# Optimization experiments

Measured on AMD Instinct MI355X. Metric: run time of the kernel, lower is better.

The kernel has to match this reference:

```python
import jax, jax.numpy as jnp
import numpy as np

STEPS = 8
TOL = 1e-6


def _kabsch(p, q):
    # p, q: [B, N, 3]; returns R [B,3,3], t [B,3] s.t. q ~= R p + t (pypose svdtf)
    pm = p.mean(axis=-2, keepdims=True)
    qm = q.mean(axis=-2, keepdims=True)
    pc = p - pm
    qc = q - qm
    H = jnp.einsum('bni,bnj->bij', pc, qc)          # 3x3 cross-covariance
    U, S, Vt = jnp.linalg.svd(H, full_matrices=False)
    V = jnp.swapaxes(Vt, -1, -2)
    Ut = jnp.swapaxes(U, -1, -2)
    d = jnp.linalg.det(jnp.matmul(V, Ut))            # reflection fix
    D = jnp.concatenate([jnp.ones(d.shape + (2,), d.dtype), d[..., None]], axis=-1)
    R = jnp.matmul(V * D[..., None, :], Ut)
    t = qm[..., 0, :] - jnp.einsum('bij,bj->bi', R, pm[..., 0, :])
    return R, t


def _rotmat_to_quat(R):
    # branchless rotation-matrix -> quaternion [qx, qy, qz, qw] (pypose order)
    r00, r11, r22 = R[..., 0, 0], R[..., 1, 1], R[..., 2, 2]
    qw = 0.5 * jnp.sqrt(jnp.clip(1.0 + r00 + r11 + r22, 1e-12))
    qx = 0.5 * jnp.sqrt(jnp.clip(1.0 + r00 - r11 - r22, 1e-12))
    qy = 0.5 * jnp.sqrt(jnp.clip(1.0 - r00 + r11 - r22, 1e-12))
    qz = 0.5 * jnp.sqrt(jnp.clip(1.0 - r00 - r11 + r22, 1e-12))
    qx = qx * jnp.where(R[..., 2, 1] - R[..., 1, 2] >= 0, 1.0, -1.0)
    qy = qy * jnp.where(R[..., 0, 2] - R[..., 2, 0] >= 0, 1.0, -1.0)
    qz = qz * jnp.where(R[..., 1, 0] - R[..., 0, 1] >= 0, 1.0, -1.0)
    return jnp.stack([qx, qy, qz, qw], axis=-1)


def _icp(psrc, ptgt):
    B = psrc.shape[0]
    tn = (ptgt * ptgt).sum(-1)                        # [B, M]

    def body(carry, _):
        pc, err, done = carry
        # brute-force 1-NN: Euclidean cdist via  |p|^2 + |q|^2 - 2 p.q
        sq = ((pc * pc).sum(-1)[:, :, None] + tn[:, None, :]
              - 2.0 * jnp.einsum('bnd,bmd->bnm', pc, ptgt))
        dist = jnp.sqrt(jnp.clip(sq, 0.0))            # [B, N, M]
        knnd = dist.min(axis=-1)                      # [B, N]
        idx = dist.argmin(axis=-1)                    # [B, N]
        errnew = knnd.mean(axis=-1)                   # [B]
        conv = jnp.all(jnp.abs(errnew - err) < TOL)
        done_new = jnp.logical_or(done, conv)
        qk = jnp.take_along_axis(ptgt, jnp.broadcast_to(idx[..., None], pc.shape), axis=1)
        R, t = _kabsch(pc, qk)
        pcnew = jnp.einsum('bij,bnj->bni', R, pc) + t[:, None, :]
        pc = jnp.where(done_new, pc, pcnew)
        err = jnp.where(done_new, err, errnew)
        return (pc, err, done_new), None

    init = (psrc, jnp.zeros((B,), psrc.dtype), jnp.array(False))
    (pc, _, _), _ = jax.lax.scan(body, init, None, length=STEPS)
    R, t = _kabsch(psrc, pc)                          # final fit psrc -> moved cloud
    quat = _rotmat_to_quat(R)
    return jnp.concatenate([t, quat], axis=-1)        # SE3 7-vector [t, qx,qy,qz,qw]


def setup_inputs() -> dict:
    key = jax.random.key(0)
    k1, k2 = jax.random.split(key)
    psrc = jax.random.normal(k1, (2, 4096, 3), dtype=jnp.float32)
    ptgt = jax.random.normal(k2, (2, 4096, 3), dtype=jnp.float32)
    return {"psrc": psrc, "ptgt": ptgt}


def reference(psrc, ptgt):
    return _icp(psrc, ptgt)
```

## Files before the change

### kernel.cpp

```cpp
#include <hip/hip_runtime.h>
#include <math.h>

#define NPTS 4096
#define MPTS 4096
#define NSTEPS 8
#define ICP_TOL 1e-6f
#define NBLK 512
#define NSUB 32

#define ACC_OFF 32768
#define CTR_OFF 98304
#define CTR_STRIDE 1536

__global__ void init_kernel(const float* __restrict__ ptgt, float* __restrict__ ws) {
    float* ptgt4 = ws;
    unsigned* ctrs = (unsigned*)(ws + CTR_OFF);
    int gid = blockIdx.x * 256 + threadIdx.x;
    if (gid < 2 * MPTS) {
        float x = ptgt[3 * gid + 0];
        float y = ptgt[3 * gid + 1];
        float z = ptgt[3 * gid + 2];
        float4 v;
        v.x = x; v.y = y; v.z = z;
        v.w = 0.5f * (x * x + y * y + z * z);
        ((float4*)ptgt4)[gid] = v;
    }
    for (int i = gid; i < NSTEPS * CTR_STRIDE; i += 8192) ctrs[i] = 0u;
}

__device__ __forceinline__ float frcp(float x) {
#if __has_builtin(__builtin_amdgcn_rcpf)
    return __builtin_amdgcn_rcpf(x);
#else
    return 1.f / x;
#endif
}
__device__ __forceinline__ float frsq(float x) {
#if __has_builtin(__builtin_amdgcn_rsqf)
    return __builtin_amdgcn_rsqf(x);
#else
    return 1.f / sqrtf(x);
#endif
}

#define DET3(a,b,c,d,e,f,g,h,i) \
    ((a)*((e)*(i)-(f)*(h)) - (b)*((d)*(i)-(f)*(g)) + (c)*((d)*(h)-(e)*(g)))

__device__ __forceinline__ void horn_quat(const float N[4][4], float q[4]) {
    float s = 1e-30f;
#pragma unroll
    for (int i = 0; i < 4; ++i)
#pragma unroll
        for (int j = 0; j < 4; ++j) s = fmaxf(s, fabsf(N[i][j]));
    float inv = frcp(s);
    float A[4][4], B[4][4];
#pragma unroll
    for (int i = 0; i < 4; ++i)
#pragma unroll
        for (int j = 0; j < 4; ++j) A[i][j] = N[i][j] * inv;
#pragma unroll
    for (int i = 0; i < 4; ++i)
#pragma unroll
        for (int j = i; j < 4; ++j) {
            float v = A[i][0]*A[0][j] + A[i][1]*A[1][j] + A[i][2]*A[2][j] + A[i][3]*A[3][j];
            B[i][j] = v; B[j][i] = v;
        }
    float p1 = A[0][0]+A[1][1]+A[2][2]+A[3][3];
    float p2 = B[0][0]+B[1][1]+B[2][2]+B[3][3];
    float p3 = 0.f, p4 = 0.f;
#pragma unroll
    for (int i = 0; i < 4; ++i)
#pragma unroll
        for (int j = 0; j < 4; ++j) { p3 += A[i][j]*B[i][j]; p4 += B[i][j]*B[i][j]; }
    float e1 = p1;
    float e2 = 0.5f*(e1*p1 - p2);
    float e3 = (e2*p1 - e1*p2 + p3)*(1.f/3.f);
    float e4 = 0.25f*(e3*p1 - e2*p2 + e1*p3 - p4);
    float lam = -3e38f;
#pragma unroll
    for (int i = 0; i < 4; ++i) {
        float r = A[i][i];
#pragma unroll
        for (int j = 0; j < 4; ++j) if (j != i) r += fabsf(A[i][j]);
        lam = fmaxf(lam, r);
    }
#pragma unroll
    for (int it = 0; it < 12; ++it) {
        float pv = (((lam - e1)*lam + e2)*lam - e3)*lam + e4;
        float dv = ((4.f*lam - 3.f*e1)*lam + 2.f*e2)*lam - e3;
        lam -= pv * frcp(dv);
    }
    float M[4][4];
#pragma unroll
    for (int i = 0; i < 4; ++i)
#pragma unroll
        for (int j = 0; j < 4; ++j) M[i][j] = A[i][j] - ((i == j) ? lam : 0.f);
    float C0 = DET3(M[1][1],M[1][2],M[1][3], M[2][1],M[2][2],M[2][3], M[3][1],M[3][2],M[3][3]);
    float C1 = DET3(M[0][0],M[0][2],M[0][3], M[2][0],M[2][2],M[2][3], M[3][0],M[3][2],M[3][3]);
    float C2 = DET3(M[0][0],M[0][1],M[0][3], M[1][0],M[1][1],M[1][3], M[3][0],M[3][1],M[3][3]);
    float C3 = DET3(M[0][0],M[0][1],M[0][2], M[1][0],M[1][1],M[1][2], M[2][0],M[2][1],M[2][2]);
    int is = 0; float cb = fabsf(C0);
    if (fabsf(C1) > cb) { cb = fabsf(C1); is = 1; }
    if (fabsf(C2) > cb) { cb = fabsf(C2); is = 2; }
    if (fabsf(C3) > cb) { cb = fabsf(C3); is = 3; }
    float v0, v1, v2, v3;
#define ROWCOF(a,b,c) { \
    v0 =  DET3(M[a][1],M[a][2],M[a][3], M[b][1],M[b][2],M[b][3], M[c][1],M[c][2],M[c][3]); \
    v1 = -DET3(M[a][0],M[a][2],M[a][3], M[b][0],M[b][2],M[b][3], M[c][0],M[c][2],M[c][3]); \
    v2 =  DET3(M[a][0],M[a][1],M[a][3], M[b][0],M[b][1],M[b][3], M[c][0],M[c][1],M[c][3]); \
    v3 = -DET3(M[a][0],M[a][1],M[a][2], M[b][0],M[b][1],M[b][2], M[c][0],M[c][1],M[c][2]); }
    if (is == 0)      ROWCOF(1,2,3)
    else if (is == 1) ROWCOF(0,2,3)
    else if (is == 2) ROWCOF(0,1,3)
    else              ROWCOF(0,1,2)
#undef ROWCOF
    float nr = frsq(v0*v0 + v1*v1 + v2*v2 + v3*v3);
    q[0] = v0*nr; q[1] = v1*nr; q[2] = v2*nr; q[3] = v3*nr;
}

#define FOR16(OP) OP(0) OP(1) OP(2) OP(3) OP(4) OP(5) OP(6) OP(7) \
                  OP(8) OP(9) OP(10) OP(11) OP(12) OP(13) OP(14) OP(15)

__global__ __launch_bounds__(256, 2) void icp_main(
    const float* __restrict__ psrc, float* __restrict__ ws,
    float* __restrict__ out) {

    float* ptgt4 = ws;
    float* acc = ws + ACC_OFF;
    unsigned* ctrs = (unsigned*)(ws + CTR_OFF);

    __shared__ float st[2][13];
    __shared__ unsigned keys[4][16];
    __shared__ float red[16][16];
    __shared__ float gred[16][16];
    __shared__ float asum[2][16];
    __shared__ int contflag;

    const int tid = threadIdx.x;
    const int bid = blockIdx.x;
    const int b = bid >> 8;
    const int n0 = (bid & 255) * 16;

    if (tid < 2) {
        st[tid][0] = 1.f; st[tid][1] = 0.f; st[tid][2] = 0.f;
        st[tid][3] = 0.f; st[tid][4] = 1.f; st[tid][5] = 0.f;
        st[tid][6] = 0.f; st[tid][7] = 0.f; st[tid][8] = 1.f;
        st[tid][9] = 0.f; st[tid][10] = 0.f; st[tid][11] = 0.f;
        st[tid][12] = 0.f;
    }
    __syncthreads();

    const int w = tid >> 6, lane = tid & 63;
    const int m0 = w * 1024 + lane;
    const float4* tpb = (const float4*)ptgt4 + ((size_t)b * MPTS + m0);
    const float* ps = psrc + ((size_t)b * NPTS + n0) * 3;

    for (int step = 0; step < NSTEPS; ++step) {
        float R00 = st[b][0], R01 = st[b][1], R02 = st[b][2];
        float R10 = st[b][3], R11 = st[b][4], R12 = st[b][5];
        float R20 = st[b][6], R21 = st[b][7], R22 = st[b][8];
        float t0 = st[b][9], t1 = st[b][10], t2 = st[b][11];

#define DECLP(i) float px##i, py##i, pz##i;
        FOR16(DECLP)
#undef DECLP
#define LOADP(i) { float x = ps[3*(i)], y = ps[3*(i)+1], z = ps[3*(i)+2]; \
        px##i = fmaf(R00, x, fmaf(R01, y, fmaf(R02, z, t0))); \
        py##i = fmaf(R10, x, fmaf(R11, y, fmaf(R12, z, t1))); \
        pz##i = fmaf(R20, x, fmaf(R21, y, fmaf(R22, z, t2))); }
        FOR16(LOADP)
#undef LOADP

#define DECLB(i) float bs##i = -3.0e38f; int ix##i = m0;
        FOR16(DECLB)
#undef DECLB

        float4 tc0 = tpb[0];
        float4 tc1 = tpb[64];
        int mreg = m0;
#pragma unroll
        for (int k = 0; k < 16; ++k) {
            float4 tnx = tpb[((k + 2) & 15) * 64];
            float tx = tc0.x, ty = tc0.y, tz = tc0.z, htn = tc0.w;
#define PAIR(i) { float s = fmaf(px##i, tx, fmaf(py##i, ty, fmaf(pz##i, tz, -htn))); \
            if (s > bs##i) { bs##i = s; ix##i = mreg; } }
            FOR16(PAIR)
#undef PAIR
            mreg += 64;
            tc0 = tc1;
            tc1 = tnx;
        }

        unsigned k_[16];
#define MKKEY(i) { unsigned ub = __float_as_uint(bs##i); \
        unsigned u = ((int)ub >= 0) ? (ub | 0x80000000u) : ~ub; \
        k_[i] = (u & 0xFFFFF000u) | (4095u - (unsigned)ix##i); }
        FOR16(MKKEY)
#undef MKKEY
#pragma unroll
        for (int r = 0; r < 4; ++r) {
            const int mm = 1 << r;
            const int W = 16 >> r;
            unsigned o_[16];
#pragma unroll
            for (int j = 0; j < W; ++j)
                o_[j] = (unsigned)__shfl_xor((int)k_[j], mm);
            const bool hi = (lane & mm) != 0;
#pragma unroll
            for (int j = 0; j < W / 2; ++j) {
                unsigned a = hi ? k_[j + W / 2] : k_[j];
                unsigned c = hi ? o_[j + W / 2] : o_[j];
                k_[j] = a > c ? a : c;
            }
        }
        {
            unsigned o = (unsigned)__shfl_xor((int)k_[0], 16);
            k_[0] = k_[0] > o ? k_[0] : o;
            o = (unsigned)__shfl_xor((int)k_[0], 32);
            k_[0] = k_[0] > o ? k_[0] : o;
        }
        if (lane < 16) {
            int p = ((lane & 1) << 3) | ((lane & 2) << 1) |
                    ((lane & 4) >> 1) | ((lane & 8) >> 3);
            keys[w][p] = k_[0];
        }
        __syncthreads();

        if (tid < 16) {
            unsigned key = keys[0][tid];
            unsigned k1 = keys[1][tid], k2 = keys[2][tid], k3 = keys[3][tid];
            key = key > k1 ? key : k1;
            key = key > k2 ? key : k2;
            key = key > k3 ? key : k3;
            int m = 4095 - (int)(key & 0xFFFu);
            float4 qq = ((const float4*)ptgt4)[(size_t)b * MPTS + m];
            const float* pp = psrc + ((size_t)b * NPTS + n0 + tid) * 3;
            float x = pp[0], y = pp[1], z = pp[2];
            float px = fmaf(R00, x, fmaf(R01, y, fmaf(R02, z, t0)));
            float py = fmaf(R10, x, fmaf(R11, y, fmaf(R12, z, t1)));
            float pz = fmaf(R20, x, fmaf(R21, y, fmaf(R22, z, t2)));
            float dx = px - qq.x, dy = py - qq.y, dz = pz - qq.z;
            float dist = sqrtf(dx * dx + dy * dy + dz * dz);
            red[tid][0] = px; red[tid][1] = py; red[tid][2] = pz;
            red[tid][3] = qq.x; red[tid][4] = qq.y; red[tid][5] = qq.z;
            red[tid][6] = px * qq.x;  red[tid][7] = px * qq.y;  red[tid][8] = px * qq.z;
            red[tid][9] = py * qq.x;  red[tid][10] = py * qq.y; red[tid][11] = py * qq.z;
            red[tid][12] = pz * qq.x; red[tid][13] = pz * qq.y; red[tid][14] = pz * qq.z;
            red[tid][15] = dist;
            float s = 0.f;
#pragma unroll
            for (int r = 0; r < 16; ++r) s += red[r][tid];
            __hip_atomic_store(&acc[((size_t)step * NBLK + bid) * 16 + tid], s,
                               __ATOMIC_RELAXED, __HIP_MEMORY_SCOPE_AGENT);
        }

        unsigned* stepc = ctrs + step * CTR_STRIDE;
        __syncthreads();

        if (step == NSTEPS - 1) {
            if (tid == 0) {
                unsigned* sub = stepc + (bid & (NSUB - 1)) * 16;
                unsigned old = __hip_atomic_fetch_add(sub, 1u, __ATOMIC_RELAXED,
                                                      __HIP_MEMORY_SCOPE_AGENT);
                if (old == (unsigned)(NBLK / NSUB) - 1u)
                    __hip_atomic_fetch_add(stepc + 512, 1u, __ATOMIC_RELAXED,
                                           __HIP_MEMORY_SCOPE_AGENT);
            }
            if (bid != 0) return;
            if (tid == 0) {
                while (__hip_atomic_load(stepc + 512, __ATOMIC_RELAXED,
                                         __HIP_MEMORY_SCOPE_AGENT) < (unsigned)NSUB) {
                    __builtin_amdgcn_s_sleep(1);
                }
            }
            __syncthreads();
        } else {
            if (tid == 0) {
                unsigned* sub = stepc + (bid & (NSUB - 1)) * 16;
                bool bcast = false;
                unsigned old = __hip_atomic_fetch_add(sub, 1u, __ATOMIC_RELAXED,
                                                      __HIP_MEMORY_SCOPE_AGENT);
                if (old == (unsigned)(NBLK / NSUB) - 1u) {
                    unsigned mold = __hip_atomic_fetch_add(stepc + 512, 1u,
                                        __ATOMIC_RELAXED, __HIP_MEMORY_SCOPE_AGENT);
                    if (mold == (unsigned)NSUB - 1u) {
#pragma unroll
                        for (int f = 0; f < NSUB; ++f)
                            __hip_atomic_store(stepc + 1024 + f * 16, 1u,
                                               __ATOMIC_RELAXED,
                                               __HIP_MEMORY_SCOPE_AGENT);
                        bcast = true;
                    }
                }
                if (!bcast) {
                    unsigned* myflag = stepc + 1024 + (bid & (NSUB - 1)) * 16;
                    while (__hip_atomic_load(myflag, __ATOMIC_RELAXED,
                                             __HIP_MEMORY_SCOPE_AGENT) == 0u) {
                        __builtin_amdgcn_s_sleep(1);
                    }
                }
            }
            __syncthreads();
        }

        {
            const float* accs = acc + (size_t)step * NBLK * 16;
            int c = tid & 15, g = tid >> 4;
            float ssum = 0.f;
#pragma unroll
            for (int i = 0; i < 32; ++i)
                ssum += accs[(size_t)(g * 32 + i) * 16 + c];
            gred[g][c] = ssum;
        }
        __syncthreads();
        if (tid < 32) {
            int bb = tid >> 4, c = tid & 15;
            float s = 0.f;
#pragma unroll
            for (int g = 0; g < 8; ++g) s += gred[bb * 8 + g][c];
            asum[bb][c] = s;
        }
        __syncthreads();
        if (tid == 0) {
            float err0 = asum[0][15] * (1.f / NPTS);
            float err1 = asum[1][15] * (1.f / NPTS);
            bool conv = (fabsf(err0 - st[0][12]) < ICP_TOL) &&
                        (fabsf(err1 - st[1][12]) < ICP_TOL);
            contflag = conv ? 2 : 1;
        }
        __syncthreads();
        if (contflag == 1 && tid < 2) {
            float a[16];
            for (int i = 0; i < 16; ++i) a[i] = asum[tid][i];
            const float inv_n = 1.f / NPTS;
            float pmx = a[0]*inv_n, pmy = a[1]*inv_n, pmz = a[2]*inv_n;
            float qmx = a[3]*inv_n, qmy = a[4]*inv_n, qmz = a[5]*inv_n;
            float H[3][3];
            for (int i = 0; i < 3; ++i)
                for (int j = 0; j < 3; ++j)
                    H[i][j] = a[6 + 3*i + j] - a[i]*a[3 + j]*inv_n;
            float Sxx=H[0][0], Sxy=H[0][1], Sxz=H[0][2];
            float Syx=H[1][0], Syy=H[1][1], Syz=H[1][2];
            float Szx=H[2][0], Szy=H[2][1], Szz=H[2][2];
            float Nm[4][4];
            Nm[0][0] = Sxx+Syy+Szz; Nm[0][1] = Syz-Szy;
            Nm[0][2] = Szx-Sxz;     Nm[0][3] = Sxy-Syx;
            Nm[1][1] = Sxx-Syy-Szz; Nm[1][2] = Sxy+Syx; Nm[1][3] = Szx+Sxz;
            Nm[2][2] = -Sxx+Syy-Szz; Nm[2][3] = Syz+Szy;
            Nm[3][3] = -Sxx-Syy+Szz;
            Nm[1][0]=Nm[0][1]; Nm[2][0]=Nm[0][2]; Nm[3][0]=Nm[0][3];
            Nm[2][1]=Nm[1][2]; Nm[3][1]=Nm[1][3]; Nm[3][2]=Nm[2][3];
            float qv[4];
            horn_quat(Nm, qv);
            float qw = qv[0], qx = qv[1], qy = qv[2], qz = qv[3];
            float R00n = 1.f - 2.f*(qy*qy + qz*qz);
            float R01n = 2.f*(qx*qy - qw*qz);
            float R02n = 2.f*(qx*qz + qw*qy);
            float R10n = 2.f*(qx*qy + qw*qz);
            float R11n = 1.f - 2.f*(qx*qx + qz*qz);
            float R12n = 2.f*(qy*qz - qw*qx);
            float R20n = 2.f*(qx*qz - qw*qy);
            float R21n = 2.f*(qy*qz + qw*qx);
            float R22n = 1.f - 2.f*(qx*qx + qy*qy);
            float tx = qmx - (R00n*pmx + R01n*pmy + R02n*pmz);
            float ty = qmy - (R10n*pmx + R11n*pmy + R12n*pmz);
            float tz = qmz - (R20n*pmx + R21n*pmy + R22n*pmz);
            float C00=st[tid][0], C01=st[tid][1], C02=st[tid][2];
            float C10=st[tid][3], C11=st[tid][4], C12=st[tid][5];
            float C20=st[tid][6], C21=st[tid][7], C22=st[tid][8];
            float T0=st[tid][9], T1=st[tid][10], T2=st[tid][11];
            float ns[12];
            ns[0] = R00n*C00 + R01n*C10 + R02n*C20;
            ns[1] = R00n*C01 + R01n*C11 + R02n*C21;
            ns[2] = R00n*C02 + R01n*C12 + R02n*C22;
            ns[3] = R10n*C00 + R11n*C10 + R12n*C20;
            ns[4] = R10n*C01 + R11n*C11 + R12n*C21;
            ns[5] = R10n*C02 + R11n*C12 + R12n*C22;
            ns[6] = R20n*C00 + R21n*C10 + R22n*C20;
            ns[7] = R20n*C01 + R21n*C11 + R22n*C21;
            ns[8] = R20n*C02 + R21n*C12 + R22n*C22;
            ns[9]  = R00n*T0 + R01n*T1 + R02n*T2 + tx;
            ns[10] = R10n*T0 + R11n*T1 + R12n*T2 + ty;
            ns[11] = R20n*T0 + R21n*T1 + R22n*T2 + tz;
            for (int i = 0; i < 12; ++i) st[tid][i] = ns[i];
            st[tid][12] = asum[tid][15] * (1.f / NPTS);
        }
        __syncthreads();
        if (contflag == 2) break;
    }

    if (bid == 0 && tid < 2) {
        float r00 = st[tid][0], r01 = st[tid][1], r02 = st[tid][2];
        float r10 = st[tid][3], r11 = st[tid][4], r12 = st[tid][5];
        float r20 = st[tid][6], r21 = st[tid][7], r22 = st[tid][8];
        float qw = 0.5f * sqrtf(fmaxf(1.f + r00 + r11 + r22, 1e-12f));
        float qx = 0.5f * sqrtf(fmaxf(1.f + r00 - r11 - r22, 1e-12f));
        float qy = 0.5f * sqrtf(fmaxf(1.f - r00 + r11 - r22, 1e-12f));
        float qz = 0.5f * sqrtf(fmaxf(1.f - r00 - r11 + r22, 1e-12f));
        qx = (r21 - r12 >= 0.f) ? qx : -qx;
        qy = (r02 - r20 >= 0.f) ? qy : -qy;
        qz = (r10 - r01 >= 0.f) ? qz : -qz;
        out[tid * 7 + 0] = st[tid][9];
        out[tid * 7 + 1] = st[tid][10];
        out[tid * 7 + 2] = st[tid][11];
        out[tid * 7 + 3] = qx;
        out[tid * 7 + 4] = qy;
        out[tid * 7 + 5] = qz;
        out[tid * 7 + 6] = qw;
    }
}

extern "C" void kernel_launch(void* const* d_in, const int* in_sizes, int n_in,
                              void* d_out, int out_size, void* d_ws, size_t ws_size,
                              hipStream_t stream) {
    const float* psrc = (const float*)d_in[0];
    const float* ptgt = (const float*)d_in[1];
    float* out = (float*)d_out;
    float* ws = (float*)d_ws;

    init_kernel<<<32, 256, 0, stream>>>(ptgt, ws);
    icp_main<<<NBLK, 256, 0, stream>>>(psrc, ws, out);
}
```

Before: 160.4 us.

## Per-batch pose solve per block, hoisted source loads, deeper prefetch, tree reductions

Each block now reduces only its own batch's partial sums, plus the other batch's error term for the global convergence test, and solves the Horn pose only for its own batch on one thread. Previously two threads solved both batches from a combined reduction. Source points are loaded into registers once instead of every step, the target prefetch gets one more stage, and the per-block and grid-wide reductions become two-level trees with more parallel threads. The Newton iteration count for the eigenvalue drops from 12 to 8. These changes shorten the serial tail of each step, which every block executes after the grid barrier, at the cost of extra registers and barriers and a possible small loss of eigenvalue precision.

```diff
diff --git a/kernel.cpp b/kernel.cpp
--- a/kernel.cpp
+++ b/kernel.cpp
@@ -85,7 +85,7 @@
         lam = fmaxf(lam, r);
     }
 #pragma unroll
-    for (int it = 0; it < 12; ++it) {
+    for (int it = 0; it < 8; ++it) {
         float pv = (((lam - e1)*lam + e2)*lam - e3)*lam + e4;
         float dv = ((4.f*lam - 3.f*e1)*lam + 2.f*e2)*lam - e3;
         lam -= pv * frcp(dv);
@@ -132,8 +132,14 @@
     __shared__ float st[2][13];
     __shared__ unsigned keys[4][16];
     __shared__ float red[16][16];
+    __shared__ float rq[4][16];
     __shared__ float gred[16][16];
-    __shared__ float asum[2][16];
+    __shared__ float gq[4][16];
+    __shared__ float oerr[64];
+    __shared__ float oe2[8];
+    __shared__ float asumv[16];
+    __shared__ float oerrF;
+    __shared__ float oErrPrev;
     __shared__ int contflag;
 
     const int tid = threadIdx.x;
@@ -141,12 +147,13 @@
     const int b = bid >> 8;
     const int n0 = (bid & 255) * 16;
 
-    if (tid < 2) {
-        st[tid][0] = 1.f; st[tid][1] = 0.f; st[tid][2] = 0.f;
-        st[tid][3] = 0.f; st[tid][4] = 1.f; st[tid][5] = 0.f;
-        st[tid][6] = 0.f; st[tid][7] = 0.f; st[tid][8] = 1.f;
-        st[tid][9] = 0.f; st[tid][10] = 0.f; st[tid][11] = 0.f;
-        st[tid][12] = 0.f;
+    if (tid == 0) {
+        st[b][0] = 1.f; st[b][1] = 0.f; st[b][2] = 0.f;
+        st[b][3] = 0.f; st[b][4] = 1.f; st[b][5] = 0.f;
+        st[b][6] = 0.f; st[b][7] = 0.f; st[b][8] = 1.f;
+        st[b][9] = 0.f; st[b][10] = 0.f; st[b][11] = 0.f;
+        st[b][12] = 0.f;
+        oErrPrev = 0.f;
     }
     __syncthreads();
 
@@ -154,6 +161,11 @@
     const int m0 = w * 1024 + lane;
     const float4* tpb = (const float4*)ptgt4 + ((size_t)b * MPTS + m0);
     const float* ps = psrc + ((size_t)b * NPTS + n0) * 3;
+
+    float sx[16], sy[16], sz[16];
+#define HOIST(i) { sx[i] = ps[3*(i)]; sy[i] = ps[3*(i)+1]; sz[i] = ps[3*(i)+2]; }
+    FOR16(HOIST)
+#undef HOIST
 
     for (int step = 0; step < NSTEPS; ++step) {
         float R00 = st[b][0], R01 = st[b][1], R02 = st[b][2];
@@ -164,7 +176,7 @@
 #define DECLP(i) float px##i, py##i, pz##i;
         FOR16(DECLP)
 #undef DECLP
-#define LOADP(i) { float x = ps[3*(i)], y = ps[3*(i)+1], z = ps[3*(i)+2]; \
+#define LOADP(i) { float x = sx[i], y = sy[i], z = sz[i]; \
         px##i = fmaf(R00, x, fmaf(R01, y, fmaf(R02, z, t0))); \
         py##i = fmaf(R10, x, fmaf(R11, y, fmaf(R12, z, t1))); \
         pz##i = fmaf(R20, x, fmaf(R21, y, fmaf(R22, z, t2))); }
@@ -177,10 +189,11 @@
 
         float4 tc0 = tpb[0];
         float4 tc1 = tpb[64];
+        float4 tc2 = tpb[128];
         int mreg = m0;
 #pragma unroll
         for (int k = 0; k < 16; ++k) {
-            float4 tnx = tpb[((k + 2) & 15) * 64];
+            float4 tnx = tpb[((k + 3) & 15) * 64];
             float tx = tc0.x, ty = tc0.y, tz = tc0.z, htn = tc0.w;
 #define PAIR(i) { float s = fmaf(px##i, tx, fmaf(py##i, ty, fmaf(pz##i, tz, -htn))); \
             if (s > bs##i) { bs##i = s; ix##i = mreg; } }
@@ -188,7 +201,8 @@
 #undef PAIR
             mreg += 64;
             tc0 = tc1;
-            tc1 = tnx;
+            tc1 = tc2;
+            tc2 = tnx;
         }
 
         unsigned k_[16];
@@ -247,9 +261,15 @@
             red[tid][9] = py * qq.x;  red[tid][10] = py * qq.y; red[tid][11] = py * qq.z;
             red[tid][12] = pz * qq.x; red[tid][13] = pz * qq.y; red[tid][14] = pz * qq.z;
             red[tid][15] = dist;
-            float s = 0.f;
-#pragma unroll
-            for (int r = 0; r < 16; ++r) s += red[r][tid];
+        }
+        __syncthreads();
+        if (tid < 64) {
+            int c = tid & 15, q = tid >> 4;
+            rq[q][c] = ((red[4*q][c] + red[4*q+1][c]) + red[4*q+2][c]) + red[4*q+3][c];
+        }
+        __syncthreads();
+        if (tid < 16) {
+            float s = ((rq[0][tid] + rq[1][tid]) + rq[2][tid]) + rq[3][tid];
             __hip_atomic_store(&acc[((size_t)step * NBLK + bid) * 16 + tid], s,
                                __ATOMIC_RELAXED, __HIP_MEMORY_SCOPE_AGENT);
         }
@@ -266,7 +286,7 @@
                     __hip_atomic_fetch_add(stepc + 512, 1u, __ATOMIC_RELAXED,
                                            __HIP_MEMORY_SCOPE_AGENT);
             }
-            if (bid != 0) return;
+            if (bid != 0 && bid != 256) return;
             if (tid == 0) {
                 while (__hip_atomic_load(stepc + 512, __ATOMIC_RELAXED,
                                          __HIP_MEMORY_SCOPE_AGENT) < (unsigned)NSUB) {
@@ -304,95 +324,115 @@
         }
 
         {
-            const float* accs = acc + (size_t)step * NBLK * 16;
+            const float* accs = acc + ((size_t)step * NBLK + b * 256) * 16;
             int c = tid & 15, g = tid >> 4;
             float ssum = 0.f;
 #pragma unroll
-            for (int i = 0; i < 32; ++i)
-                ssum += accs[(size_t)(g * 32 + i) * 16 + c];
+            for (int i = 0; i < 16; ++i)
+                ssum += accs[(size_t)(g * 16 + i) * 16 + c];
             gred[g][c] = ssum;
         }
-        __syncthreads();
-        if (tid < 32) {
-            int bb = tid >> 4, c = tid & 15;
+        if (tid >= 192) {
+            const float* acco = acc + ((size_t)step * NBLK + (1 - b) * 256) * 16;
+            int j = tid - 192;
+            float s = ((acco[(size_t)(j*4+0)*16+15] + acco[(size_t)(j*4+1)*16+15])
+                       + acco[(size_t)(j*4+2)*16+15]) + acco[(size_t)(j*4+3)*16+15];
+            oerr[j] = s;
+        }
+        __syncthreads();
+        if (tid < 64) {
+            int c = tid & 15, q = tid >> 4;
+            gq[q][c] = ((gred[4*q][c] + gred[4*q+1][c]) + gred[4*q+2][c]) + gred[4*q+3][c];
+        } else if (tid >= 64 && tid < 72) {
+            int j = tid - 64;
             float s = 0.f;
 #pragma unroll
-            for (int g = 0; g < 8; ++g) s += gred[bb * 8 + g][c];
-            asum[bb][c] = s;
-        }
-        __syncthreads();
+            for (int i = 0; i < 8; ++i) s += oerr[8*j + i];
+            oe2[j] = s;
+        }
+        __syncthreads();
+        if (tid < 16) {
+            asumv[tid] = ((gq[0][tid] + gq[1][tid]) + gq[2][tid]) + gq[3][tid];
+        } else if (tid == 16) {
+            float s = 0.f;
+#pragma unroll
+            for (int i = 0; i < 8; ++i) s += oe2[i];
+            oerrF = s;
+        }
+        __syncthreads();
+
         if (tid == 0) {
-            float err0 = asum[0][15] * (1.f / NPTS);
-            float err1 = asum[1][15] * (1.f / NPTS);
-            bool conv = (fabsf(err0 - st[0][12]) < ICP_TOL) &&
-                        (fabsf(err1 - st[1][12]) < ICP_TOL);
+            const float inv_n = 1.f / NPTS;
+            float errmy = asumv[15] * inv_n;
+            float erro  = oerrF * inv_n;
+            bool conv = (fabsf(errmy - st[b][12]) < ICP_TOL) &&
+                        (fabsf(erro - oErrPrev) < ICP_TOL);
             contflag = conv ? 2 : 1;
-        }
-        __syncthreads();
-        if (contflag == 1 && tid < 2) {
-            float a[16];
-            for (int i = 0; i < 16; ++i) a[i] = asum[tid][i];
-            const float inv_n = 1.f / NPTS;
-            float pmx = a[0]*inv_n, pmy = a[1]*inv_n, pmz = a[2]*inv_n;
-            float qmx = a[3]*inv_n, qmy = a[4]*inv_n, qmz = a[5]*inv_n;
-            float H[3][3];
-            for (int i = 0; i < 3; ++i)
-                for (int j = 0; j < 3; ++j)
-                    H[i][j] = a[6 + 3*i + j] - a[i]*a[3 + j]*inv_n;
-            float Sxx=H[0][0], Sxy=H[0][1], Sxz=H[0][2];
-            float Syx=H[1][0], Syy=H[1][1], Syz=H[1][2];
-            float Szx=H[2][0], Szy=H[2][1], Szz=H[2][2];
-            float Nm[4][4];
-            Nm[0][0] = Sxx+Syy+Szz; Nm[0][1] = Syz-Szy;
-            Nm[0][2] = Szx-Sxz;     Nm[0][3] = Sxy-Syx;
-            Nm[1][1] = Sxx-Syy-Szz; Nm[1][2] = Sxy+Syx; Nm[1][3] = Szx+Sxz;
-            Nm[2][2] = -Sxx+Syy-Szz; Nm[2][3] = Syz+Szy;
-            Nm[3][3] = -Sxx-Syy+Szz;
-            Nm[1][0]=Nm[0][1]; Nm[2][0]=Nm[0][2]; Nm[3][0]=Nm[0][3];
-            Nm[2][1]=Nm[1][2]; Nm[3][1]=Nm[1][3]; Nm[3][2]=Nm[2][3];
-            float qv[4];
-            horn_quat(Nm, qv);
-            float qw = qv[0], qx = qv[1], qy = qv[2], qz = qv[3];
-            float R00n = 1.f - 2.f*(qy*qy + qz*qz);
-            float R01n = 2.f*(qx*qy - qw*qz);
-            float R02n = 2.f*(qx*qz + qw*qy);
-            float R10n = 2.f*(qx*qy + qw*qz);
-            float R11n = 1.f - 2.f*(qx*qx + qz*qz);
-            float R12n = 2.f*(qy*qz - qw*qx);
-            float R20n = 2.f*(qx*qz - qw*qy);
-            float R21n = 2.f*(qy*qz + qw*qx);
-            float R22n = 1.f - 2.f*(qx*qx + qy*qy);
-            float tx = qmx - (R00n*pmx + R01n*pmy + R02n*pmz);
-            float ty = qmy - (R10n*pmx + R11n*pmy + R12n*pmz);
-            float tz = qmz - (R20n*pmx + R21n*pmy + R22n*pmz);
-            float C00=st[tid][0], C01=st[tid][1], C02=st[tid][2];
-            float C10=st[tid][3], C11=st[tid][4], C12=st[tid][5];
-            float C20=st[tid][6], C21=st[tid][7], C22=st[tid][8];
-            float T0=st[tid][9], T1=st[tid][10], T2=st[tid][11];
-            float ns[12];
-            ns[0] = R00n*C00 + R01n*C10 + R02n*C20;
-            ns[1] = R00n*C01 + R01n*C11 + R02n*C21;
-            ns[2] = R00n*C02 + R01n*C12 + R02n*C22;
-            ns[3] = R10n*C00 + R11n*C10 + R12n*C20;
-            ns[4] = R10n*C01 + R11n*C11 + R12n*C21;
-            ns[5] = R10n*C02 + R11n*C12 + R12n*C22;
-            ns[6] = R20n*C00 + R21n*C10 + R22n*C20;
-            ns[7] = R20n*C01 + R21n*C11 + R22n*C21;
-            ns[8] = R20n*C02 + R21n*C12 + R22n*C22;
-            ns[9]  = R00n*T0 + R01n*T1 + R02n*T2 + tx;
-            ns[10] = R10n*T0 + R11n*T1 + R12n*T2 + ty;
-            ns[11] = R20n*T0 + R21n*T1 + R22n*T2 + tz;
-            for (int i = 0; i < 12; ++i) st[tid][i] = ns[i];
-            st[tid][12] = asum[tid][15] * (1.f / NPTS);
+            if (!conv) {
+                float a[16];
+                for (int i = 0; i < 16; ++i) a[i] = asumv[i];
+                float pmx = a[0]*inv_n, pmy = a[1]*inv_n, pmz = a[2]*inv_n;
+                float qmx = a[3]*inv_n, qmy = a[4]*inv_n, qmz = a[5]*inv_n;
+                float H[3][3];
+                for (int i = 0; i < 3; ++i)
+                    for (int j = 0; j < 3; ++j)
+                        H[i][j] = a[6 + 3*i + j] - a[i]*a[3 + j]*inv_n;
+                float Sxx=H[0][0], Sxy=H[0][1], Sxz=H[0][2];
+                float Syx=H[1][0], Syy=H[1][1], Syz=H[1][2];
+                float Szx=H[2][0], Szy=H[2][1], Szz=H[2][2];
+                float Nm[4][4];
+                Nm[0][0] = Sxx+Syy+Szz; Nm[0][1] = Syz-Szy;
+                Nm[0][2] = Szx-Sxz;     Nm[0][3] = Sxy-Syx;
+                Nm[1][1] = Sxx-Syy-Szz; Nm[1][2] = Sxy+Syx; Nm[1][3] = Szx+Sxz;
+                Nm[2][2] = -Sxx+Syy-Szz; Nm[2][3] = Syz+Szy;
+                Nm[3][3] = -Sxx-Syy+Szz;
+                Nm[1][0]=Nm[0][1]; Nm[2][0]=Nm[0][2]; Nm[3][0]=Nm[0][3];
+                Nm[2][1]=Nm[1][2]; Nm[3][1]=Nm[1][3]; Nm[3][2]=Nm[2][3];
+                float qv[4];
+                horn_quat(Nm, qv);
+                float qw = qv[0], qx = qv[1], qy = qv[2], qz = qv[3];
+                float R00n = 1.f - 2.f*(qy*qy + qz*qz);
+                float R01n = 2.f*(qx*qy - qw*qz);
+                float R02n = 2.f*(qx*qz + qw*qy);
+                float R10n = 2.f*(qx*qy + qw*qz);
+                float R11n = 1.f - 2.f*(qx*qx + qz*qz);
+                float R12n = 2.f*(qy*qz - qw*qx);
+                float R20n = 2.f*(qx*qz - qw*qy);
+                float R21n = 2.f*(qy*qz + qw*qx);
+                float R22n = 1.f - 2.f*(qx*qx + qy*qy);
+                float tx = qmx - (R00n*pmx + R01n*pmy + R02n*pmz);
+                float ty = qmy - (R10n*pmx + R11n*pmy + R12n*pmz);
+                float tz = qmz - (R20n*pmx + R21n*pmy + R22n*pmz);
+                float C00=st[b][0], C01=st[b][1], C02=st[b][2];
+                float C10=st[b][3], C11=st[b][4], C12=st[b][5];
+                float C20=st[b][6], C21=st[b][7], C22=st[b][8];
+                float T0=st[b][9], T1=st[b][10], T2=st[b][11];
+                float ns[12];
+                ns[0] = R00n*C00 + R01n*C10 + R02n*C20;
+                ns[1] = R00n*C01 + R01n*C11 + R02n*C21;
+                ns[2] = R00n*C02 + R01n*C12 + R02n*C22;
+                ns[3] = R10n*C00 + R11n*C10 + R12n*C20;
+                ns[4] = R10n*C01 + R11n*C11 + R12n*C21;
+                ns[5] = R10n*C02 + R11n*C12 + R12n*C22;
+                ns[6] = R20n*C00 + R21n*C10 + R22n*C20;
+                ns[7] = R20n*C01 + R21n*C11 + R22n*C21;
+                ns[8] = R20n*C02 + R21n*C12 + R22n*C22;
+                ns[9]  = R00n*T0 + R01n*T1 + R02n*T2 + tx;
+                ns[10] = R10n*T0 + R11n*T1 + R12n*T2 + ty;
+                ns[11] = R20n*T0 + R21n*T1 + R22n*T2 + tz;
+                for (int i = 0; i < 12; ++i) st[b][i] = ns[i];
+                st[b][12] = errmy;
+                oErrPrev = erro;
+            }
         }
         __syncthreads();
         if (contflag == 2) break;
     }
 
-    if (bid == 0 && tid < 2) {
-        float r00 = st[tid][0], r01 = st[tid][1], r02 = st[tid][2];
-        float r10 = st[tid][3], r11 = st[tid][4], r12 = st[tid][5];
-        float r20 = st[tid][6], r21 = st[tid][7], r22 = st[tid][8];
+    if ((bid == 0 || bid == 256) && tid == 0) {
+        float r00 = st[b][0], r01 = st[b][1], r02 = st[b][2];
+        float r10 = st[b][3], r11 = st[b][4], r12 = st[b][5];
+        float r20 = st[b][6], r21 = st[b][7], r22 = st[b][8];
         float qw = 0.5f * sqrtf(fmaxf(1.f + r00 + r11 + r22, 1e-12f));
         float qx = 0.5f * sqrtf(fmaxf(1.f + r00 - r11 - r22, 1e-12f));
         float qy = 0.5f * sqrtf(fmaxf(1.f - r00 + r11 - r22, 1e-12f));
@@ -400,13 +440,13 @@
         qx = (r21 - r12 >= 0.f) ? qx : -qx;
         qy = (r02 - r20 >= 0.f) ? qy : -qy;
         qz = (r10 - r01 >= 0.f) ? qz : -qz;
-        out[tid * 7 + 0] = st[tid][9];
-        out[tid * 7 + 1] = st[tid][10];
-        out[tid * 7 + 2] = st[tid][11];
-        out[tid * 7 + 3] = qx;
-        out[tid * 7 + 4] = qy;
-        out[tid * 7 + 5] = qz;
-        out[tid * 7 + 6] = qw;
+        out[b * 7 + 0] = st[b][9];
+        out[b * 7 + 1] = st[b][10];
+        out[b * 7 + 2] = st[b][11];
+        out[b * 7 + 3] = qx;
+        out[b * 7 + 4] = qy;
+        out[b * 7 + 5] = qz;
+        out[b * 7 + 6] = qw;
     }
 }
 
```

Result: slower. 179.9 us (+12.1%).
